# Kernel tuning notes

Measured on AMD Instinct MI355X. Metric: run time of the kernel, lower is better.

The kernel has to match this reference:

```python
import jax, jax.numpy as jnp
import numpy as np

H = 1024   # hidden_dim
L = 2      # n_layers
B = 50     # batch (hardcoded via positions expand)
S = 457    # coords length (hardcoded arange)
T = 32     # maxlen['txt']
V = 27     # dict_size


def gru_cell(x, h, Wih, Whh, bih, bhh):
    # PyTorch GRU cell math. x: (B, in), h: (B, H)
    gi = x @ Wih.T + bih
    gh = h @ Whh.T + bhh
    ir, iz, inn = jnp.split(gi, 3, axis=-1)
    hr, hz, hn = jnp.split(gh, 3, axis=-1)
    r = jax.nn.sigmoid(ir + hr)
    z = jax.nn.sigmoid(iz + hz)
    n = jnp.tanh(inn + r * hn)
    return (1.0 - z) * n + z * h


def setup_inputs() -> dict:
    key = jax.random.key(0)
    ks = iter(jax.random.split(key, 32))
    p = lambda shape: jax.random.normal(next(ks), shape, dtype=jnp.float32) * 0.05
    inp = {
        'x': jax.random.normal(next(ks), (B, 2, S), dtype=jnp.float32),
        'emb': p((V, H)),
        # encoder GRU (layer0 input=3, layer1 input=H)
        'enc_Wih0': p((3 * H, 3)), 'enc_Whh0': p((3 * H, H)),
        'enc_bih0': p((3 * H,)),   'enc_bhh0': p((3 * H,)),
        'enc_Wih1': p((3 * H, H)), 'enc_Whh1': p((3 * H, H)),
        'enc_bih1': p((3 * H,)),   'enc_bhh1': p((3 * H,)),
        # decoder GRU, stacked over layers (all inputs are H)
        'dec_Wih': p((L, 3 * H, H)), 'dec_Whh': p((L, 3 * H, H)),
        'dec_bih': p((L, 3 * H)),    'dec_bhh': p((L, 3 * H)),
        # attention_fc: Linear(2H, H) + ReLU ; fc: Linear(H, V)
        'attn_W': p((H, 2 * H)), 'attn_b': p((H,)),
        'fc_W': p((V, H)),       'fc_b': p((V,)),
    }
    return inp


def reference(x, emb, enc_Wih0, enc_Whh0, enc_bih0, enc_bhh0,
              enc_Wih1, enc_Whh1, enc_bih1, enc_bhh1,
              dec_Wih, dec_Whh, dec_bih, dec_bhh,
              attn_W, attn_b, fc_W, fc_b):
    # ----- encoder -----
    pos = jnp.broadcast_to(jnp.arange(S, dtype=x.dtype)[None, :, None], (B, S, 1))
    inp = jnp.concatenate([jnp.transpose(x, (0, 2, 1)), pos], axis=-1)  # (B,S,3)
    seq = jnp.transpose(inp, (1, 0, 2))  # (S,B,3) time-major for scan
    h0 = jnp.zeros((B, H), x.dtype)
    hiddens = []
    for (Wih, Whh, bih, bhh) in ((enc_Wih0, enc_Whh0, enc_bih0, enc_bhh0),
                                 (enc_Wih1, enc_Whh1, enc_bih1, enc_bhh1)):
        def step(h, xt, Wih=Wih, Whh=Whh, bih=bih, bhh=bhh):
            h2 = gru_cell(xt, h, Wih, Whh, bih, bhh)
            return h2, h2
        hT, seq = jax.lax.scan(step, h0, seq)
        hiddens.append(hT)
    enc_outs = jnp.transpose(seq, (1, 0, 2))  # (B,S,H)
    hidden = jnp.stack(hiddens)               # (L,B,H)

    def dec_step(carry, _):
        vec_in, hid = carry
        x_t = emb[vec_in]  # (B,H)
        new_h = []
        inp_t = x_t
        for l in range(L):
            hl = gru_cell(inp_t, hid[l], dec_Wih[l], dec_Whh[l], dec_bih[l], dec_bhh[l])
            new_h.append(hl)
            inp_t = hl
        out_t = inp_t  # (B,H)
        score = jnp.einsum('bsh,bh->bs', enc_outs, out_t)      # bmm(v, q)
        w = jax.nn.softmax(score, axis=1)                      # softmax over S
        a = jnp.einsum('bsh,bs->bh', enc_outs, w)              # bmm(v^T, w)
        comb = jnp.concatenate([out_t, a], axis=-1)            # (B,2H)
        hfc = jax.nn.relu(comb @ attn_W.T + attn_b)
        logits = hfc @ fc_W.T + fc_b                           # (B,V)
        nv = jnp.argmax(logits, axis=-1).astype(jnp.int32)
        return (nv, jnp.stack(new_h)), (logits, w)

    init = (jnp.zeros((B,), jnp.int32), hidden)
    (_, hid_f), (logits_seq, w_seq) = jax.lax.scan(dec_step, init, None, length=T)
    vec_out = jnp.transpose(logits_seq, (1, 0, 2))  # (B,T,V)
    attn_w = jnp.transpose(w_seq, (1, 2, 0))        # (B,S,T)
    return vec_out, hid_f, attn_w
```

## Files before the change

kernel.cpp:

```cpp
#include <hip/hip_runtime.h>
#include <math.h>

#define HD 1024
#define BB 50
#define SS 457
#define TT 32
#define VV 27
#define C3 3072

#define TC 64
#define LP 68

__global__ __launch_bounds__(256) void gemm_part_kernel(
    const float* __restrict__ A0, const float* __restrict__ W0,
    const float* __restrict__ A1, const float* __restrict__ W1,
    int K, int C, int nks, float* __restrict__ gpart,
    int gatherZ1, const int* __restrict__ tok, const float* __restrict__ emb)
{
  const int z = blockIdx.z;
  const float* A = z ? A1 : A0;
  const float* W = z ? W1 : W0;
  float* outp = gpart + (size_t)z * (size_t)nks * BB * C;
  const int kper = K / nks;
  const int k0 = blockIdx.y * kper;
  const int c0 = blockIdx.x * TC;

  __shared__ __align__(16) float As[16][LP];
  __shared__ __align__(16) float Ws[16][LP];

  const int tid = threadIdx.x;
  const int tx = tid & 15, ty = tid >> 4;
  float acc[4][4] = {{0.f}};

  for (int kk = 0; kk < kper; kk += 16) {
#pragma unroll
    for (int i = 0; i < 4; i++) {
      int e = tid + i * 256;
      int bb = e >> 4, kl = e & 15;
      float va = 0.f;
      if (bb < BB) {
        const float* arow;
        if (gatherZ1 && z == 1) arow = emb + (size_t)tok[bb] * HD;
        else                    arow = A + (size_t)bb * K;
        va = arow[k0 + kk + kl];
      }
      As[kl][bb] = va;
      int cc = c0 + bb;
      Ws[kl][bb] = W[(size_t)cc * K + k0 + kk + kl];
    }
    __syncthreads();
#pragma unroll
    for (int kl = 0; kl < 16; kl++) {
      const float4 a4 = *(const float4*)&As[kl][ty << 2];
      const float4 w4 = *(const float4*)&Ws[kl][tx << 2];
      float av[4] = {a4.x, a4.y, a4.z, a4.w};
      float wv[4] = {w4.x, w4.y, w4.z, w4.w};
#pragma unroll
      for (int i = 0; i < 4; i++)
#pragma unroll
        for (int j = 0; j < 4; j++)
          acc[i][j] += av[i] * wv[j];
    }
    __syncthreads();
  }

#pragma unroll
  for (int i = 0; i < 4; i++) {
    int b = (ty << 2) + i;
    if (b >= BB) continue;
    float* orow = outp + ((size_t)blockIdx.y * BB + b) * C + c0 + (tx << 2);
#pragma unroll
    for (int j = 0; j < 4; j++) orow[j] = acc[i][j];
  }
}

__global__ __launch_bounds__(256) void gru_gate_kernel(
    const float* __restrict__ gpart, int C, int nks, int ihFromPart,
    const float* __restrict__ Wih0, const float* __restrict__ x, int t,
    const float* __restrict__ bih, const float* __restrict__ bhh,
    float* __restrict__ h, float* __restrict__ seq_out, int seq_stride)
{
  int tid = blockIdx.x * 256 + threadIdx.x;
  if (tid >= BB * HD) return;
  int b = tid >> 10, j = tid & 1023;

  float ghr = 0.f, ghz = 0.f, ghn = 0.f;
  for (int ks = 0; ks < nks; ks++) {
    const float* row = gpart + ((size_t)ks * BB + b) * C;
    ghr += row[j]; ghz += row[HD + j]; ghn += row[2 * HD + j];
  }
  float gir = 0.f, giz = 0.f, gin = 0.f;
  if (ihFromPart) {
    const float* g1 = gpart + (size_t)nks * BB * C;
    for (int ks = 0; ks < nks; ks++) {
      const float* row = g1 + ((size_t)ks * BB + b) * C;
      gir += row[j]; giz += row[HD + j]; gin += row[2 * HD + j];
    }
  } else {
    float x0 = x[(size_t)b * 2 * SS + t];
    float x1 = x[(size_t)b * 2 * SS + SS + t];
    float pp = (float)t;
    const float* wr = Wih0 + (size_t)j * 3;
    const float* wz = Wih0 + (size_t)(HD + j) * 3;
    const float* wn = Wih0 + (size_t)(2 * HD + j) * 3;
    gir = wr[0] * x0 + wr[1] * x1 + wr[2] * pp;
    giz = wz[0] * x0 + wz[1] * x1 + wz[2] * pp;
    gin = wn[0] * x0 + wn[1] * x1 + wn[2] * pp;
  }
  gir += bih[j];      giz += bih[HD + j];      gin += bih[2 * HD + j];
  ghr += bhh[j];      ghz += bhh[HD + j];      ghn += bhh[2 * HD + j];

  float r  = 1.f / (1.f + expf(-(gir + ghr)));
  float zg = 1.f / (1.f + expf(-(giz + ghz)));
  float n  = tanhf(gin + r * ghn);
  float hv = h[tid];
  float hn2 = (1.f - zg) * n + zg * hv;
  h[tid] = hn2;
  if (seq_out) seq_out[(size_t)b * seq_stride + j] = hn2;
}

__global__ __launch_bounds__(256) void score_kernel(
    const float* __restrict__ enc, const float* __restrict__ q,
    float* __restrict__ sc)
{
  int gw = (blockIdx.x * 256 + threadIdx.x) >> 6;
  int lane = threadIdx.x & 63;
  if (gw >= BB * SS) return;
  int b = gw / SS, s = gw - b * SS;
  const float* e = enc + ((size_t)s * BB + b) * HD;
  const float* qq = q + (size_t)b * HD;
  float acc = 0.f;
#pragma unroll
  for (int i = 0; i < 16; i++) acc += e[lane + 64 * i] * qq[lane + 64 * i];
  for (int off = 32; off; off >>= 1) acc += __shfl_down(acc, off);
  if (lane == 0) sc[b * SS + s] = acc;
}

__global__ __launch_bounds__(512) void softmax_attn_kernel(
    const float* __restrict__ sc, float* __restrict__ w,
    float* __restrict__ attn_out, int t)
{
  int b = blockIdx.x;
  __shared__ float red[512];
  float m = -1e30f;
  for (int s = threadIdx.x; s < SS; s += 512) m = fmaxf(m, sc[b * SS + s]);
  red[threadIdx.x] = m; __syncthreads();
  for (int o = 256; o; o >>= 1) {
    if (threadIdx.x < o) red[threadIdx.x] = fmaxf(red[threadIdx.x], red[threadIdx.x + o]);
    __syncthreads();
  }
  m = red[0]; __syncthreads();
  float sum = 0.f;
  for (int s = threadIdx.x; s < SS; s += 512) sum += expf(sc[b * SS + s] - m);
  red[threadIdx.x] = sum; __syncthreads();
  for (int o = 256; o; o >>= 1) {
    if (threadIdx.x < o) red[threadIdx.x] += red[threadIdx.x + o];
    __syncthreads();
  }
  float inv = 1.f / red[0];
  for (int s = threadIdx.x; s < SS; s += 512) {
    float v = expf(sc[b * SS + s] - m) * inv;
    w[b * SS + s] = v;
    attn_out[((size_t)b * SS + s) * TT + t] = v;
  }
}

__global__ __launch_bounds__(256) void amix_kernel(
    const float* __restrict__ enc, const float* __restrict__ w,
    float* __restrict__ comb)
{
  int tid = blockIdx.x * 256 + threadIdx.x;
  if (tid >= BB * HD) return;
  int b = tid >> 10, j = tid & 1023;
  const float* wb = w + b * SS;
  float acc = 0.f;
#pragma unroll 4
  for (int s = 0; s < SS; s++) acc += wb[s] * enc[((size_t)s * BB + b) * HD + j];
  comb[(size_t)b * 2048 + HD + j] = acc;
}

__global__ __launch_bounds__(256) void fcrelu_kernel(
    const float* __restrict__ gpart, int nks,
    const float* __restrict__ bias, float* __restrict__ hfc)
{
  int tid = blockIdx.x * 256 + threadIdx.x;
  if (tid >= BB * HD) return;
  int b = tid >> 10, i = tid & 1023;
  float acc = bias[i];
  for (int ks = 0; ks < nks; ks++) acc += gpart[((size_t)ks * BB + b) * HD + i];
  hfc[tid] = fmaxf(acc, 0.f);
}

__global__ __launch_bounds__(256) void logits_kernel(
    const float* __restrict__ hfc, const float* __restrict__ fcW,
    const float* __restrict__ fcb, float* __restrict__ outv, int t)
{
  int gw = (blockIdx.x * 256 + threadIdx.x) >> 6;
  int lane = threadIdx.x & 63;
  if (gw >= BB * VV) return;
  int b = gw / VV, v = gw - b * VV;
  const float* hb = hfc + (size_t)b * HD;
  const float* wv = fcW + (size_t)v * HD;
  float acc = 0.f;
#pragma unroll
  for (int i = 0; i < 16; i++) acc += hb[lane + 64 * i] * wv[lane + 64 * i];
  for (int off = 32; off; off >>= 1) acc += __shfl_down(acc, off);
  if (lane == 0) outv[((size_t)b * TT + t) * VV + v] = acc + fcb[v];
}

__global__ __launch_bounds__(64) void argmax_kernel(
    const float* __restrict__ outv, int t, int* __restrict__ tok)
{
  int b = threadIdx.x;
  if (b >= BB) return;
  const float* l = outv + ((size_t)b * TT + t) * VV;
  float best = l[0]; int bi = 0;
  for (int v = 1; v < VV; v++) { float xv = l[v]; if (xv > best) { best = xv; bi = v; } }
  tok[b] = bi;
}

__global__ __launch_bounds__(256) void init_kernel(
    float* __restrict__ h0, float* __restrict__ h1, int* __restrict__ tok)
{
  int tid = blockIdx.x * 256 + threadIdx.x;
  if (tid < BB * HD) { h0[tid] = 0.f; h1[tid] = 0.f; }
  if (tid < BB) tok[tid] = 0;
}

__global__ __launch_bounds__(256) void hidcopy_kernel(
    const float* __restrict__ h0, const float* __restrict__ h1,
    float* __restrict__ outh)
{
  int tid = blockIdx.x * 256 + threadIdx.x;
  if (tid >= BB * HD) return;
  outh[tid] = h0[tid];
  outh[BB * HD + tid] = h1[tid];
}

extern "C" void kernel_launch(void* const* d_in, const int* in_sizes, int n_in,
                              void* d_out, int out_size, void* d_ws, size_t ws_size,
                              hipStream_t stream)
{
  const float* x     = (const float*)d_in[0];
  const float* emb   = (const float*)d_in[1];
  const float* eWih0 = (const float*)d_in[2];
  const float* eWhh0 = (const float*)d_in[3];
  const float* ebih0 = (const float*)d_in[4];
  const float* ebhh0 = (const float*)d_in[5];
  const float* eWih1 = (const float*)d_in[6];
  const float* eWhh1 = (const float*)d_in[7];
  const float* ebih1 = (const float*)d_in[8];
  const float* ebhh1 = (const float*)d_in[9];
  const float* dWih  = (const float*)d_in[10];
  const float* dWhh  = (const float*)d_in[11];
  const float* dbih  = (const float*)d_in[12];
  const float* dbhh  = (const float*)d_in[13];
  const float* attnW = (const float*)d_in[14];
  const float* attnB = (const float*)d_in[15];
  const float* fcW   = (const float*)d_in[16];
  const float* fcB   = (const float*)d_in[17];
  float* out = (float*)d_out;

  float* ws     = (float*)d_ws;
  float* h0     = ws;
  float* h1     = h0 + BB * HD;
  float* gpart  = h1 + BB * HD;
  float* enc    = gpart + 16 * BB * C3;
  float* comb   = enc + (size_t)SS * BB * HD;
  float* scoreb = comb + BB * 2048;
  float* wsm    = scoreb + BB * SS;
  float* hfc    = wsm + BB * SS;
  int*   tok    = (int*)(hfc + BB * HD);

  float* out_vec  = out;
  float* out_hid  = out + BB * TT * VV;
  float* out_attn = out_hid + 2 * BB * HD;

  init_kernel<<<200, 256, 0, stream>>>(h0, h1, tok);

  for (int t = 0; t < SS; t++) {
    gemm_part_kernel<<<dim3(C3 / TC, 16, 1), 256, 0, stream>>>(
        h0, eWhh0, nullptr, nullptr, HD, C3, 16, gpart, 0, nullptr, nullptr);
    gru_gate_kernel<<<200, 256, 0, stream>>>(
        gpart, C3, 16, 0, eWih0, x, t, ebih0, ebhh0, h0, nullptr, 0);
    gemm_part_kernel<<<dim3(C3 / TC, 8, 2), 256, 0, stream>>>(
        h1, eWhh1, h0, eWih1, HD, C3, 8, gpart, 0, nullptr, nullptr);
    gru_gate_kernel<<<200, 256, 0, stream>>>(
        gpart, C3, 8, 1, nullptr, nullptr, 0, ebih1, ebhh1, h1,
        enc + (size_t)t * BB * HD, HD);
  }

  for (int t = 0; t < TT; t++) {
    gemm_part_kernel<<<dim3(C3 / TC, 8, 2), 256, 0, stream>>>(
        h0, dWhh, nullptr, dWih, HD, C3, 8, gpart, 1, tok, emb);
    gru_gate_kernel<<<200, 256, 0, stream>>>(
        gpart, C3, 8, 1, nullptr, nullptr, 0, dbih, dbhh, h0, nullptr, 0);
    gemm_part_kernel<<<dim3(C3 / TC, 8, 2), 256, 0, stream>>>(
        h1, dWhh + (size_t)C3 * HD, h0, dWih + (size_t)C3 * HD,
        HD, C3, 8, gpart, 0, nullptr, nullptr);
    gru_gate_kernel<<<200, 256, 0, stream>>>(
        gpart, C3, 8, 1, nullptr, nullptr, 0, dbih + C3, dbhh + C3, h1,
        comb, 2048);

    score_kernel<<<(BB * SS * 64 + 255) / 256, 256, 0, stream>>>(enc, h1, scoreb);
    softmax_attn_kernel<<<BB, 512, 0, stream>>>(scoreb, wsm, out_attn, t);
    amix_kernel<<<200, 256, 0, stream>>>(enc, wsm, comb);

    gemm_part_kernel<<<dim3(HD / TC, 16, 1), 256, 0, stream>>>(
        comb, attnW, nullptr, nullptr, 2 * HD, HD, 16, gpart, 0, nullptr, nullptr);
    fcrelu_kernel<<<200, 256, 0, stream>>>(gpart, 16, attnB, hfc);
    logits_kernel<<<(BB * VV * 64 + 255) / 256, 256, 0, stream>>>(
        hfc, fcW, fcB, out_vec, t);
    argmax_kernel<<<1, 64, 0, stream>>>(out_vec, t, tok);
  }

  hidcopy_kernel<<<200, 256, 0, stream>>>(h0, h1, out_hid);
}
```

Baseline: 27.50 ms.

## Fuse GEMV and GRU gates into one wavefront-skewed kernel per step

Replaces the split-K GEMM plus separate gate kernels with a single rowdot kernel that computes matvec rows and applies the GRU gate epilogue in-block, removing the partial-sum round trips through global memory. The encoder layers are skewed so layer0 step p and layer1 step p-1 run in one launch with double-buffered hidden states, roughly halving encoder launches. The decoder precomputes layer1's Whh product alongside layer0, and it fuses softmax with the attention mix and logits with argmax. The cost is a complex multi-mode kernel with 1024-thread blocks streaming weights directly from global memory, which could limit occupancy or coalescing.

```diff
diff --git a/kernel.cpp b/kernel.cpp
--- a/kernel.cpp
+++ b/kernel.cpp
@@ -6,121 +6,232 @@
 #define SS 457
 #define TT 32
 #define VV 27
-#define C3 3072
-
-#define TC 64
-#define LP 68
-
-__global__ __launch_bounds__(256) void gemm_part_kernel(
-    const float* __restrict__ A0, const float* __restrict__ W0,
-    const float* __restrict__ A1, const float* __restrict__ W1,
-    int K, int C, int nks, float* __restrict__ gpart,
-    int gatherZ1, const int* __restrict__ tok, const float* __restrict__ emb)
-{
-  const int z = blockIdx.z;
-  const float* A = z ? A1 : A0;
-  const float* W = z ? W1 : W0;
-  float* outp = gpart + (size_t)z * (size_t)nks * BB * C;
-  const int kper = K / nks;
-  const int k0 = blockIdx.y * kper;
-  const int c0 = blockIdx.x * TC;
-
-  __shared__ __align__(16) float As[16][LP];
-  __shared__ __align__(16) float Ws[16][LP];
+
+#define KC 64
+#define HSTR 68
+
+template<int RPG>
+__global__ __launch_bounds__(1024) void rowdot_kernel(
+    int mode, int p,
+    const float* __restrict__ Ws,
+    const float* __restrict__ srcS,
+    const float* __restrict__ bihS, const float* __restrict__ bhhS,
+    const float* __restrict__ hvS,
+    float* __restrict__ outS,
+    const float* __restrict__ Wgi, const float* __restrict__ Wgh,
+    const float* __restrict__ srcGI, const float* __restrict__ srcGH,
+    const float* __restrict__ bihD, const float* __restrict__ bhhD,
+    const float* __restrict__ hvD,
+    float* __restrict__ outD, float* __restrict__ encD,
+    const float* __restrict__ x, const float* __restrict__ Wih0,
+    const float* __restrict__ emb, const int* __restrict__ tok,
+    const float* __restrict__ scr_r, float* __restrict__ scr_w,
+    float* __restrict__ comb)
+{
+  __shared__ __align__(16) float hs[2][64][HSTR];
+  __shared__ float acc2[2][36][64];
 
   const int tid = threadIdx.x;
-  const int tx = tid & 15, ty = tid >> 4;
-  float acc[4][4] = {{0.f}};
-
-  for (int kk = 0; kk < kper; kk += 16) {
-#pragma unroll
-    for (int i = 0; i < 4; i++) {
-      int e = tid + i * 256;
-      int bb = e >> 4, kl = e & 15;
-      float va = 0.f;
-      if (bb < BB) {
-        const float* arow;
-        if (gatherZ1 && z == 1) arow = emb + (size_t)tok[bb] * HD;
-        else                    arow = A + (size_t)bb * K;
-        va = arow[k0 + kk + kl];
+  const int blk = blockIdx.x;
+
+  bool isDual; int j0; int K; int gateType; int gather = 0;
+  const float* W0 = nullptr; const float* W1 = nullptr;
+  const float* sA = nullptr; const float* sB = nullptr;
+
+  if (mode == 0) {
+    if (blk < 86) {
+      if (p == 457) return;
+      isDual = false; j0 = blk * 12; K = 1024; gateType = 0; W0 = Ws; sA = srcS;
+    } else {
+      if (p == 0) return;
+      isDual = true; j0 = (blk - 86) * 6; K = 1024; gateType = 1;
+      W0 = Wgi; W1 = Wgh; sA = srcGI; sB = srcGH;
+    }
+  } else if (mode == 1) {
+    if (blk < 171) {
+      isDual = true; j0 = blk * 6; K = 1024; gateType = 1; gather = 1;
+      W0 = Wgi; W1 = Wgh; sA = srcGI; sB = srcGH;
+    } else {
+      isDual = false; j0 = (blk - 171) * 12; K = 1024; gateType = 2; W0 = Ws; sA = srcS;
+    }
+  } else if (mode == 2) {
+    isDual = false; j0 = blk * 12; K = 1024; gateType = 3; W0 = Ws; sA = srcS;
+  } else {
+    isDual = false; j0 = blk * 12; K = 2048; gateType = 4; W0 = Ws; sA = srcS;
+  }
+
+  const int wv = __builtin_amdgcn_readfirstlane(tid >> 6);
+  const int lane = tid & 63;
+  const int rg = wv & 3, kh = wv >> 2;
+  const int srcsel = isDual ? (rg >> 1) : 0;
+
+  const float* wp[RPG];
+#pragma unroll
+  for (int rr = 0; rr < RPG; ++rr) {
+    int lr = rg * RPG + rr;
+    int wrow;
+    if (gateType == 4) {
+      wrow = j0 + lr; if (wrow > 1023) wrow = 1023;
+    } else if (isDual) {
+      int lr2 = (rg & 1) * RPG + rr;
+      int g = lr2 / 6, jl = lr2 % 6;
+      int j = j0 + jl; if (j > 1023) j = 1023;
+      wrow = g * 1024 + j;
+    } else {
+      int g = lr / 12, jl = lr % 12;
+      int j = j0 + jl; if (j > 1023) j = 1023;
+      wrow = g * 1024 + j;
+    }
+    const float* Wsel = (isDual && (rg >> 1)) ? W1 : W0;
+    wp[rr] = Wsel + (size_t)wrow * K;
+  }
+
+  const int nst = isDual ? 1600 : 800;
+  const int nch = K / KC;
+
+  auto rowp = [&](int sel, int b) -> const float* {
+    if (sel) return sB + (size_t)b * K;
+    if (gather) return emb + (size_t)tok[b] * HD;
+    return sA + (size_t)b * K;
+  };
+
+  float4 pre0 = make_float4(0.f, 0.f, 0.f, 0.f);
+  float4 pre1 = make_float4(0.f, 0.f, 0.f, 0.f);
+
+  if (tid < nst) { int sel = tid >= 800; int e = tid - (sel ? 800 : 0);
+                   pre0 = *(const float4*)(rowp(sel, e >> 4) + (e & 15) * 4); }
+  if (isDual && tid + 1024 < nst) { int e = tid + 224;
+                   pre1 = *(const float4*)(rowp(1, e >> 4) + (e & 15) * 4); }
+
+  float acc[RPG];
+#pragma unroll
+  for (int r = 0; r < RPG; ++r) acc[r] = 0.f;
+
+  for (int c = 0; c < nch; ++c) {
+    const int kb = c * KC;
+    __syncthreads();
+    if (tid < nst) { int sel = tid >= 800; int e = tid - (sel ? 800 : 0);
+                     *(float4*)&hs[sel][e >> 4][(e & 15) * 4] = pre0; }
+    if (isDual && tid + 1024 < nst) { int e = tid + 224;
+                     *(float4*)&hs[1][e >> 4][(e & 15) * 4] = pre1; }
+    __syncthreads();
+    if (c + 1 < nch) {
+      const int kb2 = kb + KC;
+      if (tid < nst) { int sel = tid >= 800; int e = tid - (sel ? 800 : 0);
+                       pre0 = *(const float4*)(rowp(sel, e >> 4) + kb2 + (e & 15) * 4); }
+      if (isDual && tid + 1024 < nst) { int e = tid + 224;
+                       pre1 = *(const float4*)(rowp(1, e >> 4) + kb2 + (e & 15) * 4); }
+    }
+#pragma unroll
+    for (int g4 = 0; g4 < 4; ++g4) {
+      const int ko = kh * 16 + g4 * 4;
+      const float4 hv = *(const float4*)&hs[srcsel][lane][ko];
+#pragma unroll
+      for (int rr = 0; rr < RPG; ++rr) {
+        const float4 w4 = *(const float4*)(wp[rr] + kb + ko);
+        acc[rr] = fmaf(hv.x, w4.x, acc[rr]);
+        acc[rr] = fmaf(hv.y, w4.y, acc[rr]);
+        acc[rr] = fmaf(hv.z, w4.z, acc[rr]);
+        acc[rr] = fmaf(hv.w, w4.w, acc[rr]);
       }
-      As[kl][bb] = va;
-      int cc = c0 + bb;
-      Ws[kl][bb] = W[(size_t)cc * K + k0 + kk + kl];
-    }
-    __syncthreads();
-#pragma unroll
-    for (int kl = 0; kl < 16; kl++) {
-      const float4 a4 = *(const float4*)&As[kl][ty << 2];
-      const float4 w4 = *(const float4*)&Ws[kl][tx << 2];
-      float av[4] = {a4.x, a4.y, a4.z, a4.w};
-      float wv[4] = {w4.x, w4.y, w4.z, w4.w};
-#pragma unroll
-      for (int i = 0; i < 4; i++)
-#pragma unroll
-        for (int j = 0; j < 4; j++)
-          acc[i][j] += av[i] * wv[j];
-    }
-    __syncthreads();
-  }
-
-#pragma unroll
-  for (int i = 0; i < 4; i++) {
-    int b = (ty << 2) + i;
-    if (b >= BB) continue;
-    float* orow = outp + ((size_t)blockIdx.y * BB + b) * C + c0 + (tx << 2);
-#pragma unroll
-    for (int j = 0; j < 4; j++) orow[j] = acc[i][j];
-  }
-}
-
-__global__ __launch_bounds__(256) void gru_gate_kernel(
-    const float* __restrict__ gpart, int C, int nks, int ihFromPart,
-    const float* __restrict__ Wih0, const float* __restrict__ x, int t,
-    const float* __restrict__ bih, const float* __restrict__ bhh,
-    float* __restrict__ h, float* __restrict__ seq_out, int seq_stride)
-{
-  int tid = blockIdx.x * 256 + threadIdx.x;
-  if (tid >= BB * HD) return;
-  int b = tid >> 10, j = tid & 1023;
-
-  float ghr = 0.f, ghz = 0.f, ghn = 0.f;
-  for (int ks = 0; ks < nks; ks++) {
-    const float* row = gpart + ((size_t)ks * BB + b) * C;
-    ghr += row[j]; ghz += row[HD + j]; ghn += row[2 * HD + j];
-  }
-  float gir = 0.f, giz = 0.f, gin = 0.f;
-  if (ihFromPart) {
-    const float* g1 = gpart + (size_t)nks * BB * C;
-    for (int ks = 0; ks < nks; ks++) {
-      const float* row = g1 + ((size_t)ks * BB + b) * C;
-      gir += row[j]; giz += row[HD + j]; gin += row[2 * HD + j];
+    }
+  }
+
+  if (kh < 2) {
+#pragma unroll
+    for (int rr = 0; rr < RPG; ++rr) acc2[kh][rg * RPG + rr][lane] = acc[rr];
+  }
+  __syncthreads();
+  if (kh >= 2) {
+#pragma unroll
+    for (int rr = 0; rr < RPG; ++rr) acc2[kh - 2][rg * RPG + rr][lane] += acc[rr];
+  }
+  __syncthreads();
+
+  if (gateType == 0) {
+    if (tid < 600) {
+      int jl = tid / 50, b = tid - jl * 50;
+      int j = j0 + jl;
+      if (j < 1024) {
+        float ghr = acc2[0][jl][b]    + acc2[1][jl][b]    + bhhS[j];
+        float ghz = acc2[0][12+jl][b] + acc2[1][12+jl][b] + bhhS[1024 + j];
+        float ghn = acc2[0][24+jl][b] + acc2[1][24+jl][b] + bhhS[2048 + j];
+        float x0 = x[b * 914 + p], x1 = x[b * 914 + 457 + p], pp = (float)p;
+        const float* w3r = Wih0 + (size_t)j * 3;
+        const float* w3z = Wih0 + (size_t)(1024 + j) * 3;
+        const float* w3n = Wih0 + (size_t)(2048 + j) * 3;
+        float gir = w3r[0]*x0 + w3r[1]*x1 + w3r[2]*pp + bihS[j];
+        float giz = w3z[0]*x0 + w3z[1]*x1 + w3z[2]*pp + bihS[1024 + j];
+        float gin = w3n[0]*x0 + w3n[1]*x1 + w3n[2]*pp + bihS[2048 + j];
+        float r = 1.f / (1.f + expf(-(gir + ghr)));
+        float z = 1.f / (1.f + expf(-(giz + ghz)));
+        float n = tanhf(gin + r * ghn);
+        float hv = hvS[b * 1024 + j];
+        outS[b * 1024 + j] = (1.f - z) * n + z * hv;
+      }
+    }
+  } else if (gateType == 1) {
+    if (tid < 300) {
+      int jl = tid / 50, b = tid - jl * 50;
+      int j = j0 + jl;
+      if (j < 1024) {
+        float gir = acc2[0][jl][b]    + acc2[1][jl][b]    + bihD[j];
+        float giz = acc2[0][6+jl][b]  + acc2[1][6+jl][b]  + bihD[1024 + j];
+        float gin = acc2[0][12+jl][b] + acc2[1][12+jl][b] + bihD[2048 + j];
+        float ghr = acc2[0][18+jl][b] + acc2[1][18+jl][b] + bhhD[j];
+        float ghz = acc2[0][24+jl][b] + acc2[1][24+jl][b] + bhhD[1024 + j];
+        float ghn = acc2[0][30+jl][b] + acc2[1][30+jl][b] + bhhD[2048 + j];
+        float r = 1.f / (1.f + expf(-(gir + ghr)));
+        float z = 1.f / (1.f + expf(-(giz + ghz)));
+        float n = tanhf(gin + r * ghn);
+        float hv = hvD[b * 1024 + j];
+        float h2 = (1.f - z) * n + z * hv;
+        outD[b * 1024 + j] = h2;
+        if (mode == 0) encD[b * 1024 + j] = h2;
+      }
+    }
+  } else if (gateType == 2) {
+    for (int e2 = tid; e2 < 1800; e2 += 1024) {
+      int lr = e2 / 50, b = e2 - lr * 50;
+      int g = lr / 12, jl = lr - g * 12;
+      int j = j0 + jl;
+      if (j < 1024)
+        scr_w[(size_t)(g * 1024 + j) * 64 + b] = acc2[0][lr][b] + acc2[1][lr][b];
+    }
+  } else if (gateType == 3) {
+    if (tid < 600) {
+      int jl = tid / 50, b = tid - jl * 50;
+      int j = j0 + jl;
+      if (j < 1024) {
+        float gir = acc2[0][jl][b]    + acc2[1][jl][b]    + bihS[j];
+        float giz = acc2[0][12+jl][b] + acc2[1][12+jl][b] + bihS[1024 + j];
+        float gin = acc2[0][24+jl][b] + acc2[1][24+jl][b] + bihS[2048 + j];
+        float ghr = scr_r[(size_t)j * 64 + b]          + bhhS[j];
+        float ghz = scr_r[(size_t)(1024 + j) * 64 + b] + bhhS[1024 + j];
+        float ghn = scr_r[(size_t)(2048 + j) * 64 + b] + bhhS[2048 + j];
+        float r = 1.f / (1.f + expf(-(gir + ghr)));
+        float z = 1.f / (1.f + expf(-(giz + ghz)));
+        float n = tanhf(gin + r * ghn);
+        float hv = hvS[b * 1024 + j];
+        float h2 = (1.f - z) * n + z * hv;
+        outS[b * 1024 + j] = h2;
+        comb[b * 2048 + j] = h2;
+      }
     }
   } else {
-    float x0 = x[(size_t)b * 2 * SS + t];
-    float x1 = x[(size_t)b * 2 * SS + SS + t];
-    float pp = (float)t;
-    const float* wr = Wih0 + (size_t)j * 3;
-    const float* wz = Wih0 + (size_t)(HD + j) * 3;
-    const float* wn = Wih0 + (size_t)(2 * HD + j) * 3;
-    gir = wr[0] * x0 + wr[1] * x1 + wr[2] * pp;
-    giz = wz[0] * x0 + wz[1] * x1 + wz[2] * pp;
-    gin = wn[0] * x0 + wn[1] * x1 + wn[2] * pp;
-  }
-  gir += bih[j];      giz += bih[HD + j];      gin += bih[2 * HD + j];
-  ghr += bhh[j];      ghz += bhh[HD + j];      ghn += bhh[2 * HD + j];
-
-  float r  = 1.f / (1.f + expf(-(gir + ghr)));
-  float zg = 1.f / (1.f + expf(-(giz + ghz)));
-  float n  = tanhf(gin + r * ghn);
-  float hv = h[tid];
-  float hn2 = (1.f - zg) * n + zg * hv;
-  h[tid] = hn2;
-  if (seq_out) seq_out[(size_t)b * seq_stride + j] = hn2;
+    if (tid < 600) {
+      int lr = tid / 50, b = tid - lr * 50;
+      int o = j0 + lr;
+      if (o < 1024) {
+        float v = acc2[0][lr][b] + acc2[1][lr][b] + bihS[o];
+        outS[b * 1024 + o] = fmaxf(v, 0.f);
+      }
+    }
+  }
 }
 
 __global__ __launch_bounds__(256) void score_kernel(
-    const float* __restrict__ enc, const float* __restrict__ q,
+    const float* __restrict__ enc, const float* __restrict__ comb,
     float* __restrict__ sc)
 {
   int gw = (blockIdx.x * 256 + threadIdx.x) >> 6;
@@ -128,113 +239,86 @@
   if (gw >= BB * SS) return;
   int b = gw / SS, s = gw - b * SS;
   const float* e = enc + ((size_t)s * BB + b) * HD;
-  const float* qq = q + (size_t)b * HD;
-  float acc = 0.f;
-#pragma unroll
-  for (int i = 0; i < 16; i++) acc += e[lane + 64 * i] * qq[lane + 64 * i];
-  for (int off = 32; off; off >>= 1) acc += __shfl_down(acc, off);
-  if (lane == 0) sc[b * SS + s] = acc;
-}
-
-__global__ __launch_bounds__(512) void softmax_attn_kernel(
-    const float* __restrict__ sc, float* __restrict__ w,
-    float* __restrict__ attn_out, int t)
-{
-  int b = blockIdx.x;
-  __shared__ float red[512];
+  const float* q = comb + (size_t)b * 2048;
+  float a = 0.f;
+#pragma unroll
+  for (int i = 0; i < 16; i++) a += e[lane + 64 * i] * q[lane + 64 * i];
+  for (int off = 32; off; off >>= 1) a += __shfl_down(a, off);
+  if (!lane) sc[b * SS + s] = a;
+}
+
+__global__ __launch_bounds__(256) void softmax_amix_kernel(
+    const float* __restrict__ sc, const float* __restrict__ enc,
+    float* __restrict__ comb, float* __restrict__ attn_out, int t)
+{
+  __shared__ float w[SS];
+  __shared__ float red[256];
+  int blk = blockIdx.x; int b = blk / 5, sl = blk - b * 5;
+  int tid = threadIdx.x;
   float m = -1e30f;
-  for (int s = threadIdx.x; s < SS; s += 512) m = fmaxf(m, sc[b * SS + s]);
-  red[threadIdx.x] = m; __syncthreads();
-  for (int o = 256; o; o >>= 1) {
-    if (threadIdx.x < o) red[threadIdx.x] = fmaxf(red[threadIdx.x], red[threadIdx.x + o]);
-    __syncthreads();
-  }
+  for (int s = tid; s < SS; s += 256) { float v = sc[b * SS + s]; w[s] = v; m = fmaxf(m, v); }
+  red[tid] = m; __syncthreads();
+  for (int o = 128; o; o >>= 1) { if (tid < o) red[tid] = fmaxf(red[tid], red[tid + o]); __syncthreads(); }
   m = red[0]; __syncthreads();
   float sum = 0.f;
-  for (int s = threadIdx.x; s < SS; s += 512) sum += expf(sc[b * SS + s] - m);
-  red[threadIdx.x] = sum; __syncthreads();
-  for (int o = 256; o; o >>= 1) {
-    if (threadIdx.x < o) red[threadIdx.x] += red[threadIdx.x + o];
-    __syncthreads();
-  }
+  for (int s = tid; s < SS; s += 256) { float e = expf(w[s] - m); w[s] = e; sum += e; }
+  red[tid] = sum; __syncthreads();
+  for (int o = 128; o; o >>= 1) { if (tid < o) red[tid] += red[tid + o]; __syncthreads(); }
   float inv = 1.f / red[0];
-  for (int s = threadIdx.x; s < SS; s += 512) {
-    float v = expf(sc[b * SS + s] - m) * inv;
-    w[b * SS + s] = v;
-    attn_out[((size_t)b * SS + s) * TT + t] = v;
-  }
-}
-
-__global__ __launch_bounds__(256) void amix_kernel(
-    const float* __restrict__ enc, const float* __restrict__ w,
-    float* __restrict__ comb)
-{
-  int tid = blockIdx.x * 256 + threadIdx.x;
-  if (tid >= BB * HD) return;
-  int b = tid >> 10, j = tid & 1023;
-  const float* wb = w + b * SS;
-  float acc = 0.f;
+  __syncthreads();
+  for (int s = tid; s < SS; s += 256) w[s] *= inv;
+  __syncthreads();
+  if (sl == 0)
+    for (int s = tid; s < SS; s += 256) attn_out[((size_t)b * SS + s) * TT + t] = w[s];
+  int j0 = sl * 208; int jl = min(208, 1024 - j0);
+  if (tid < jl) {
+    int j = j0 + tid; float a = 0.f;
 #pragma unroll 4
-  for (int s = 0; s < SS; s++) acc += wb[s] * enc[((size_t)s * BB + b) * HD + j];
-  comb[(size_t)b * 2048 + HD + j] = acc;
-}
-
-__global__ __launch_bounds__(256) void fcrelu_kernel(
-    const float* __restrict__ gpart, int nks,
-    const float* __restrict__ bias, float* __restrict__ hfc)
-{
-  int tid = blockIdx.x * 256 + threadIdx.x;
-  if (tid >= BB * HD) return;
-  int b = tid >> 10, i = tid & 1023;
-  float acc = bias[i];
-  for (int ks = 0; ks < nks; ks++) acc += gpart[((size_t)ks * BB + b) * HD + i];
-  hfc[tid] = fmaxf(acc, 0.f);
-}
-
-__global__ __launch_bounds__(256) void logits_kernel(
+    for (int s = 0; s < SS; s++) a += w[s] * enc[((size_t)s * BB + b) * HD + j];
+    comb[(size_t)b * 2048 + HD + j] = a;
+  }
+}
+
+__global__ __launch_bounds__(256) void logits_argmax_kernel(
     const float* __restrict__ hfc, const float* __restrict__ fcW,
-    const float* __restrict__ fcb, float* __restrict__ outv, int t)
-{
-  int gw = (blockIdx.x * 256 + threadIdx.x) >> 6;
-  int lane = threadIdx.x & 63;
-  if (gw >= BB * VV) return;
-  int b = gw / VV, v = gw - b * VV;
+    const float* __restrict__ fcb, float* __restrict__ outv, int t,
+    int* __restrict__ tok)
+{
+  __shared__ float lg[32];
+  int b = blockIdx.x, tid = threadIdx.x;
+  int wv = tid >> 6, lane = tid & 63;
   const float* hb = hfc + (size_t)b * HD;
-  const float* wv = fcW + (size_t)v * HD;
-  float acc = 0.f;
-#pragma unroll
-  for (int i = 0; i < 16; i++) acc += hb[lane + 64 * i] * wv[lane + 64 * i];
-  for (int off = 32; off; off >>= 1) acc += __shfl_down(acc, off);
-  if (lane == 0) outv[((size_t)b * TT + t) * VV + v] = acc + fcb[v];
-}
-
-__global__ __launch_bounds__(64) void argmax_kernel(
-    const float* __restrict__ outv, int t, int* __restrict__ tok)
-{
-  int b = threadIdx.x;
-  if (b >= BB) return;
-  const float* l = outv + ((size_t)b * TT + t) * VV;
-  float best = l[0]; int bi = 0;
-  for (int v = 1; v < VV; v++) { float xv = l[v]; if (xv > best) { best = xv; bi = v; } }
-  tok[b] = bi;
-}
-
-__global__ __launch_bounds__(256) void init_kernel(
-    float* __restrict__ h0, float* __restrict__ h1, int* __restrict__ tok)
-{
-  int tid = blockIdx.x * 256 + threadIdx.x;
-  if (tid < BB * HD) { h0[tid] = 0.f; h1[tid] = 0.f; }
-  if (tid < BB) tok[tid] = 0;
+  for (int v = wv; v < VV; v += 4) {
+    const float* wr = fcW + (size_t)v * HD;
+    float a = 0.f;
+#pragma unroll
+    for (int i = 0; i < 16; i++) a += hb[lane + 64 * i] * wr[lane + 64 * i];
+    for (int off = 32; off; off >>= 1) a += __shfl_down(a, off);
+    if (!lane) lg[v] = a + fcb[v];
+  }
+  __syncthreads();
+  if (tid == 0) {
+    float best = lg[0]; int bi = 0;
+    for (int v = 1; v < VV; v++) { if (lg[v] > best) { best = lg[v]; bi = v; } }
+    tok[b] = bi;
+  }
+  if (tid < VV) outv[((size_t)b * TT + t) * VV + tid] = lg[tid];
+}
+
+__global__ __launch_bounds__(256) void init_kernel(float* __restrict__ hbufs,
+                                                   int* __restrict__ tok)
+{
+  int i = blockIdx.x * 256 + threadIdx.x;
+  if (i < 204800) hbufs[i] = 0.f;
+  if (i < BB) tok[i] = 0;
 }
 
 __global__ __launch_bounds__(256) void hidcopy_kernel(
     const float* __restrict__ h0, const float* __restrict__ h1,
     float* __restrict__ outh)
 {
-  int tid = blockIdx.x * 256 + threadIdx.x;
-  if (tid >= BB * HD) return;
-  outh[tid] = h0[tid];
-  outh[BB * HD + tid] = h1[tid];
+  int i = blockIdx.x * 256 + threadIdx.x;
+  if (i < 51200) { outh[i] = h0[i]; outh[51200 + i] = h1[i]; }
 }
 
 extern "C" void kernel_launch(void* const* d_in, const int* in_sizes, int n_in,
@@ -261,58 +345,65 @@
   const float* fcB   = (const float*)d_in[17];
   float* out = (float*)d_out;
 
-  float* ws     = (float*)d_ws;
-  float* h0     = ws;
-  float* h1     = h0 + BB * HD;
-  float* gpart  = h1 + BB * HD;
-  float* enc    = gpart + 16 * BB * C3;
-  float* comb   = enc + (size_t)SS * BB * HD;
+  float* ws = (float*)d_ws;
+  float* h0b[2] = { ws,          ws + 51200 };
+  float* h1b[2] = { ws + 102400, ws + 153600 };
+  float* enc    = ws + 204800;
+  float* scr    = enc + (size_t)SS * BB * HD;
+  float* comb   = scr + 3072 * 64;
   float* scoreb = comb + BB * 2048;
-  float* wsm    = scoreb + BB * SS;
-  float* hfc    = wsm + BB * SS;
+  float* hfc    = scoreb + BB * SS;
   int*   tok    = (int*)(hfc + BB * HD);
 
   float* out_vec  = out;
   float* out_hid  = out + BB * TT * VV;
   float* out_attn = out_hid + 2 * BB * HD;
 
-  init_kernel<<<200, 256, 0, stream>>>(h0, h1, tok);
-
-  for (int t = 0; t < SS; t++) {
-    gemm_part_kernel<<<dim3(C3 / TC, 16, 1), 256, 0, stream>>>(
-        h0, eWhh0, nullptr, nullptr, HD, C3, 16, gpart, 0, nullptr, nullptr);
-    gru_gate_kernel<<<200, 256, 0, stream>>>(
-        gpart, C3, 16, 0, eWih0, x, t, ebih0, ebhh0, h0, nullptr, 0);
-    gemm_part_kernel<<<dim3(C3 / TC, 8, 2), 256, 0, stream>>>(
-        h1, eWhh1, h0, eWih1, HD, C3, 8, gpart, 0, nullptr, nullptr);
-    gru_gate_kernel<<<200, 256, 0, stream>>>(
-        gpart, C3, 8, 1, nullptr, nullptr, 0, ebih1, ebhh1, h1,
-        enc + (size_t)t * BB * HD, HD);
-  }
-
-  for (int t = 0; t < TT; t++) {
-    gemm_part_kernel<<<dim3(C3 / TC, 8, 2), 256, 0, stream>>>(
-        h0, dWhh, nullptr, dWih, HD, C3, 8, gpart, 1, tok, emb);
-    gru_gate_kernel<<<200, 256, 0, stream>>>(
-        gpart, C3, 8, 1, nullptr, nullptr, 0, dbih, dbhh, h0, nullptr, 0);
-    gemm_part_kernel<<<dim3(C3 / TC, 8, 2), 256, 0, stream>>>(
-        h1, dWhh + (size_t)C3 * HD, h0, dWih + (size_t)C3 * HD,
-        HD, C3, 8, gpart, 0, nullptr, nullptr);
-    gru_gate_kernel<<<200, 256, 0, stream>>>(
-        gpart, C3, 8, 1, nullptr, nullptr, 0, dbih + C3, dbhh + C3, h1,
-        comb, 2048);
-
-    score_kernel<<<(BB * SS * 64 + 255) / 256, 256, 0, stream>>>(enc, h1, scoreb);
-    softmax_attn_kernel<<<BB, 512, 0, stream>>>(scoreb, wsm, out_attn, t);
-    amix_kernel<<<200, 256, 0, stream>>>(enc, wsm, comb);
-
-    gemm_part_kernel<<<dim3(HD / TC, 16, 1), 256, 0, stream>>>(
-        comb, attnW, nullptr, nullptr, 2 * HD, HD, 16, gpart, 0, nullptr, nullptr);
-    fcrelu_kernel<<<200, 256, 0, stream>>>(gpart, 16, attnB, hfc);
-    logits_kernel<<<(BB * VV * 64 + 255) / 256, 256, 0, stream>>>(
-        hfc, fcW, fcB, out_vec, t);
-    argmax_kernel<<<1, 64, 0, stream>>>(out_vec, t, tok);
-  }
-
-  hidcopy_kernel<<<200, 256, 0, stream>>>(h0, h1, out_hid);
-}
+  const float* dWih1 = dWih + (size_t)3072 * 1024;
+  const float* dWhh1 = dWhh + (size_t)3072 * 1024;
+  const float* dbih1 = dbih + 3072;
+  const float* dbhh1 = dbhh + 3072;
+
+  init_kernel<<<800, 256, 0, stream>>>(ws, tok);
+
+  for (int p = 0; p <= 457; ++p) {
+    float* h0r = h0b[(p + 1) & 1]; float* h0w = h0b[p & 1];
+    float* h1r = h1b[p & 1];       float* h1w = h1b[(p + 1) & 1];
+    float* encp = enc + (size_t)(p > 0 ? p - 1 : 0) * BB * HD;
+    rowdot_kernel<9><<<257, 1024, 0, stream>>>(
+        0, p,
+        eWhh0, h0r, ebih0, ebhh0, h0r, h0w,
+        eWih1, eWhh1, h0r, h1r, ebih1, ebhh1, h1r, h1w, encp,
+        x, eWih0, emb, tok, nullptr, nullptr, nullptr);
+  }
+
+  for (int t = 0; t < TT; ++t) {
+    float* h0r = h0b[t & 1]; float* h0w = h0b[(t + 1) & 1];
+    float* h1r = h1b[t & 1]; float* h1w = h1b[(t + 1) & 1];
+
+    rowdot_kernel<9><<<257, 1024, 0, stream>>>(
+        1, t,
+        dWhh1, h1r, nullptr, nullptr, nullptr, nullptr,
+        dWih, dWhh, nullptr, h0r, dbih, dbhh, h0r, h0w, nullptr,
+        nullptr, nullptr, emb, tok, nullptr, scr, nullptr);
+
+    rowdot_kernel<9><<<86, 1024, 0, stream>>>(
+        2, t,
+        dWih1, h0w, dbih1, dbhh1, h1r, h1w,
+        nullptr, nullptr, nullptr, nullptr, nullptr, nullptr, nullptr, nullptr, nullptr,
+        nullptr, nullptr, emb, tok, scr, nullptr, comb);
+
+    score_kernel<<<(BB * SS * 64 + 255) / 256, 256, 0, stream>>>(enc, comb, scoreb);
+    softmax_amix_kernel<<<250, 256, 0, stream>>>(scoreb, enc, comb, out_attn, t);
+
+    rowdot_kernel<3><<<86, 1024, 0, stream>>>(
+        3, t,
+        attnW, comb, attnB, nullptr, nullptr, hfc,
+        nullptr, nullptr, nullptr, nullptr, nullptr, nullptr, nullptr, nullptr, nullptr,
+        nullptr, nullptr, emb, tok, nullptr, nullptr, nullptr);
+
+    logits_argmax_kernel<<<BB, 256, 0, stream>>>(hfc, fcW, fcB, out_vec, t, tok);
+  }
+
+  hidcopy_kernel<<<200, 256, 0, stream>>>(h0b[0], h1b[0], out_hid);
+}
```

Result: slower. 82.50 ms (+200.0%).
